# Kernel tuning notes

Measured on AMD Instinct MI355X. Metric: run time of the kernel, lower is better.

## Reference

```python
import jax, jax.numpy as jnp
import numpy as np

NEG_SLOPE = 0.2  # PyG GATConv default negative_slope
EPS = 1e-16      # PyG softmax denominator eps


def gat_layer(x, src, dst, W, a_src, a_dst, num_nodes):
    """One GATConv (eval mode, self-loops already appended to src/dst).
    x: [N, Fin], W: [Fin, H*C], a_src/a_dst: [H, C]. Returns [N, H, C]."""
    H, C = a_src.shape
    h = (x @ W).reshape(num_nodes, H, C)                  # [N,H,C]
    alpha_src = jnp.sum(h * a_src, axis=-1)               # [N,H]
    alpha_dst = jnp.sum(h * a_dst, axis=-1)               # [N,H]
    e = alpha_src[src] + alpha_dst[dst]                   # [E,H]
    e = jnp.where(e > 0, e, NEG_SLOPE * e)                # leaky_relu
    # segment softmax keyed by destination node
    m = jax.ops.segment_max(e, dst, num_segments=num_nodes)   # [N,H]
    ex = jnp.exp(e - m[dst])                              # [E,H]
    s = jax.ops.segment_sum(ex, dst, num_segments=num_nodes)  # [N,H]
    alpha = ex / (s[dst] + EPS)                           # [E,H]
    # weighted scatter-aggregation of source features
    msg = h[src] * alpha[..., None]                       # [E,H,C]
    out = jax.ops.segment_sum(msg, dst, num_segments=num_nodes)  # [N,H,C]
    return out


def setup_inputs() -> dict:
    key = jax.random.key(0)
    ks = jax.random.split(key, 10)
    N, E = 50000, 800000
    Fin, C1, H, Fout = 128, 32, 8, 1
    x = jax.random.normal(ks[0], (N, Fin), dtype=jnp.float32)
    edge_index = jax.random.randint(ks[1], (2, E), 0, N).astype(jnp.int64)
    sc = 0.1
    W1 = jax.random.normal(ks[2], (Fin, H * C1), dtype=jnp.float32) * sc
    att_src1 = jax.random.normal(ks[3], (H, C1), dtype=jnp.float32) * sc
    att_dst1 = jax.random.normal(ks[4], (H, C1), dtype=jnp.float32) * sc
    bias1 = jnp.zeros((H * C1,), dtype=jnp.float32)
    W2 = jax.random.normal(ks[5], (H * C1, Fout), dtype=jnp.float32) * sc
    att_src2 = jax.random.normal(ks[6], (1, Fout), dtype=jnp.float32) * sc
    att_dst2 = jax.random.normal(ks[7], (1, Fout), dtype=jnp.float32) * sc
    bias2 = jnp.zeros((Fout,), dtype=jnp.float32)
    return {"x": x, "edge_index": edge_index, "W1": W1, "att_src1": att_src1,
            "att_dst1": att_dst1, "bias1": bias1, "W2": W2, "att_src2": att_src2,
            "att_dst2": att_dst2, "bias2": bias2}


def reference(x, edge_index, W1, att_src1, att_dst1, bias1, W2, att_src2, att_dst2, bias2):
    N = x.shape[0]
    loops = jnp.arange(N, dtype=edge_index.dtype)
    src = jnp.concatenate([edge_index[0], loops])   # add_self_loops=True
    dst = jnp.concatenate([edge_index[1], loops])
    # layer 1: heads=8, concat=True
    h1 = gat_layer(x, src, dst, W1, att_src1, att_dst1, N)      # [N,H,C1]
    h1 = h1.reshape(N, -1) + bias1                               # [N,H*C1]
    h1 = jax.nn.elu(h1)
    # layer 2: heads=1, concat=False (single head -> identity mean)
    h2 = gat_layer(h1, src, dst, W2, att_src2, att_dst2, N)      # [N,1,1]
    h2 = h2.reshape(N, -1) + bias2                               # [N,1]
    return jax.nn.sigmoid(h2).squeeze(-1)                        # [N]
```

## Files before the change

### kernel.cpp

```cpp
#include <hip/hip_runtime.h>
#include <math.h>

#define NEG_SLOPE 0.2f
#define GAT_EPS 1e-16f
#define NEG_BIG -3.0e38f
#define LOG2E 1.4426950408889634f
#define MAXDEG 96
#define BCAP 6144
#define CHUNK 2048
#define PREPB 136

typedef __attribute__((ext_vector_type(8))) short short8;
typedef __attribute__((ext_vector_type(4))) float floatx4;

__device__ __forceinline__ float leaky(float v) {
    return v > 0.f ? v : NEG_SLOPE * v;
}
__device__ __forceinline__ unsigned short f2bf(float f) {
    unsigned u = __float_as_uint(f);
    unsigned r = u + 0x7FFFu + ((u >> 16) & 1u);
    return (unsigned short)(r >> 16);
}
__device__ __forceinline__ float bf2f(unsigned short h) {
    return __uint_as_float(((unsigned)h) << 16);
}

__global__ __launch_bounds__(256) void prep_scatterA(
    const float* __restrict__ W1, const float* __restrict__ a_src,
    const float* __restrict__ a_dst, unsigned short* __restrict__ w1t,
    const int* __restrict__ ei, unsigned int* __restrict__ bucket_buf,
    int* __restrict__ bucket_cnt, int E, int ET)
{
    __shared__ int lhist[256];
    __shared__ int lbase[256];
    const int t = threadIdx.x;

    if (blockIdx.x < PREPB) {
        int idx = blockIdx.x * 256 + t;
        if (idx < 128 * 256) {
            int n = idx >> 7, k = idx & 127;
            w1t[idx] = f2bf(W1[(size_t)k * 256 + n]);
        }
        if (idx < 2048) {
            int j = idx >> 7, k = idx & 127;
            const float* a = (j < 8) ? (a_src + j * 32) : (a_dst + (j - 8) * 32);
            const float* wr = W1 + (size_t)k * 256 + (j & 7) * 32;
            float s = 0.f;
            #pragma unroll
            for (int c = 0; c < 32; ++c) s += wr[c] * a[c];
            w1t[(size_t)(256 + j) * 128 + k] = f2bf(s);
        }
        return;
    }

    lhist[t] = 0;
    __syncthreads();
    const int base = (blockIdx.x - PREPB) * CHUNK;
    unsigned int pk[8]; int bk[8], rk[8]; bool v[8];
    #pragma unroll
    for (int k = 0; k < 8; ++k) {
        int i = base + k * 256 + t;
        v[k] = i < ET;
        int ii = v[k] ? i : 0;
        int src = (ii < E) ? ei[ii] : (ii - E);
        int dst = (ii < E) ? ei[E + ii] : (ii - E);
        bk[k] = dst >> 8;
        pk[k] = ((unsigned)src << 8) | (unsigned)(dst & 255);
    }
    #pragma unroll
    for (int k = 0; k < 8; ++k)
        if (v[k]) rk[k] = atomicAdd(&lhist[bk[k]], 1);
    __syncthreads();
    if (lhist[t] > 0) lbase[t] = atomicAdd(&bucket_cnt[t], lhist[t]);
    __syncthreads();
    #pragma unroll
    for (int k = 0; k < 8; ++k) {
        if (v[k]) {
            int pos = lbase[bk[k]] + rk[k];
            if (pos < BCAP) bucket_buf[(size_t)bk[k] * BCAP + pos] = pk[k];
        }
    }
}

__global__ __launch_bounds__(256) void gemm_scatterB(
    const float* __restrict__ x, const unsigned short* __restrict__ w1t,
    unsigned short* __restrict__ h1b, float* __restrict__ as1, float* __restrict__ ad1,
    const unsigned int* __restrict__ bucket_buf, const int* __restrict__ bucket_cnt,
    int* __restrict__ cnt, unsigned short* __restrict__ csr_pad,
    int N, int ntiles)
{
    __shared__ __align__(16) unsigned short Asl[64][40];
    __shared__ __align__(16) unsigned short Bsl[272][40];
    __shared__ int lcnt[256];
    const int t = threadIdx.x;

    if (blockIdx.x >= ntiles) {
        const int b = blockIdx.x - ntiles;
        lcnt[t] = 0;
        __syncthreads();
        int tot = bucket_cnt[b]; if (tot > BCAP) tot = BCAP;
        const unsigned int* bp = bucket_buf + (size_t)b * BCAP;
        for (int j = t; j < tot; j += 256) {
            unsigned int e = bp[j];
            int loc = e & 255;
            int src = (int)(e >> 8);
            int slot = atomicAdd(&lcnt[loc], 1);
            if (slot < MAXDEG)
                csr_pad[(((size_t)b << 8) | loc) * MAXDEG + slot] = (unsigned short)src;
        }
        __syncthreads();
        int node = (b << 8) | t;
        if (node < N) cnt[node] = lcnt[t];
        return;
    }

    const int row0 = blockIdx.x * 64;
    const int wave = t >> 6, lane = t & 63;
    const int l15 = lane & 15, quad = lane >> 4;

    floatx4 acc[17];
    #pragma unroll
    for (int i = 0; i < 17; ++i) acc[i] = (floatx4){0.f, 0.f, 0.f, 0.f};

    for (int kc = 0; kc < 128; kc += 32) {
        {
            int r = t >> 2, q = t & 3;
            int row = row0 + r; if (row > N - 1) row = N - 1;
            const float4* xp = (const float4*)(x + (size_t)row * 128 + kc + q * 8);
            float4 f0 = xp[0], f1 = xp[1];
            ushort4 u0, u1;
            u0.x = f2bf(f0.x); u0.y = f2bf(f0.y); u0.z = f2bf(f0.z); u0.w = f2bf(f0.w);
            u1.x = f2bf(f1.x); u1.y = f2bf(f1.y); u1.z = f2bf(f1.z); u1.w = f2bf(f1.w);
            *(ushort4*)&Asl[r][q * 8] = u0;
            *(ushort4*)&Asl[r][q * 8 + 4] = u1;
        }
        {
            #pragma unroll
            for (int q = 0; q < 4; ++q) {
                uint4 v = *(const uint4*)&w1t[(size_t)t * 128 + kc + q * 8];
                *(uint4*)&Bsl[t][q * 8] = v;
            }
            if (t < 16) {
                #pragma unroll
                for (int q = 0; q < 4; ++q) {
                    uint4 v = *(const uint4*)&w1t[(size_t)(256 + t) * 128 + kc + q * 8];
                    *(uint4*)&Bsl[256 + t][q * 8] = v;
                }
            }
        }
        __syncthreads();
        short8 a = *(const short8*)&Asl[wave * 16 + l15][quad * 8];
        #pragma unroll
        for (int nt = 0; nt < 17; ++nt) {
            short8 bb = *(const short8*)&Bsl[nt * 16 + l15][quad * 8];
            acc[nt] = __builtin_amdgcn_mfma_f32_16x16x32_bf16(a, bb, acc[nt], 0, 0, 0);
        }
        __syncthreads();
    }
    #pragma unroll
    for (int reg = 0; reg < 4; ++reg) {
        int row = row0 + wave * 16 + quad * 4 + reg;
        if (row < N) {
            #pragma unroll
            for (int nt = 0; nt < 16; ++nt) {
                int hh = nt >> 1, cc = ((nt & 1) << 4) + l15;
                h1b[((size_t)hh * N + row) * 32 + cc] = f2bf(acc[nt][reg]);
            }
            float vv = acc[16][reg] * LOG2E;
            if (l15 < 8) as1[(size_t)l15 * N + row] = vv;
            else         ad1[(size_t)(l15 - 8) * N + row] = vv;
        }
    }
}

__global__ __launch_bounds__(256) void aggr1_fused(
    const int* __restrict__ cnt, const unsigned short* __restrict__ csr_pad,
    const float* __restrict__ as1, const float* __restrict__ ad1,
    const unsigned short* __restrict__ h1b,
    const float* __restrict__ bias1, const float* __restrict__ W2,
    float* __restrict__ h2, int N)
{
    const int h = blockIdx.x & 7;
    const int n = (blockIdx.x >> 3) * 32 + (threadIdx.x >> 3);
    const int lane8 = threadIdx.x & 7;
    if (n >= N) return;
    const int wbase = (threadIdx.x & 63) & ~7;

    const size_t rs = (size_t)n * MAXDEG;
    int deg = cnt[n]; if (deg > MAXDEG) deg = MAXDEG;
    const float* as1h = as1 + (size_t)h * N;
    const unsigned short* h1h = h1b + ((size_t)h * N) * 32;
    float adv = ad1[(size_t)h * N + n];

    float m = NEG_BIG, s = 0.f;
    float4 acc = make_float4(0.f, 0.f, 0.f, 0.f);

    for (int j0 = 0; j0 < deg; j0 += 8) {
        bool va = (j0 + lane8) < deg;
        int sv = 0;
        if (va) sv = csr_pad[rs + j0 + lane8];
        float l = NEG_BIG;
        if (va) l = leaky(as1h[sv] + adv);
        int srcs[8];
        #pragma unroll
        for (int j = 0; j < 8; ++j) srcs[j] = __shfl(sv, wbase + j);
        uint2 hv[8];
        #pragma unroll
        for (int j = 0; j < 8; ++j)
            hv[j] = *(const uint2*)&h1h[((unsigned)srcs[j] << 5) + (lane8 << 2)];
        float lj[8];
        #pragma unroll
        for (int j = 0; j < 8; ++j) lj[j] = __shfl(l, wbase + j);
        float Mc = fmaxf(fmaxf(fmaxf(lj[0], lj[1]), fmaxf(lj[2], lj[3])),
                         fmaxf(fmaxf(lj[4], lj[5]), fmaxf(lj[6], lj[7])));
        if (__any(Mc > m + 8.f)) {
            float mn = fmaxf(m, Mc);
            float sc = exp2f(m - mn);
            s *= sc; acc.x *= sc; acc.y *= sc; acc.z *= sc; acc.w *= sc;
            m = mn;
        }
        #pragma unroll
        for (int j = 0; j < 8; ++j) {
            float p = exp2f(lj[j] - m);
            s += p;
            unsigned d0 = hv[j].x, d1 = hv[j].y;
            acc.x += p * __uint_as_float(d0 << 16);
            acc.y += p * __uint_as_float(d0 & 0xFFFF0000u);
            acc.z += p * __uint_as_float(d1 << 16);
            acc.w += p * __uint_as_float(d1 & 0xFFFF0000u);
        }
    }

    float inv = 1.f / (s + GAT_EPS);
    acc.x *= inv; acc.y *= inv; acc.z *= inv; acc.w *= inv;

    int f = h * 32 + lane8 * 4;
    float4 b = *(const float4*)&bias1[f];
    acc.x += b.x; acc.y += b.y; acc.z += b.z; acc.w += b.w;
    acc.x = acc.x > 0.f ? acc.x : __expf(acc.x) - 1.f;
    acc.y = acc.y > 0.f ? acc.y : __expf(acc.y) - 1.f;
    acc.z = acc.z > 0.f ? acc.z : __expf(acc.z) - 1.f;
    acc.w = acc.w > 0.f ? acc.w : __expf(acc.w) - 1.f;
    float4 w = *(const float4*)&W2[f];
    float part = acc.x * w.x + acc.y * w.y + acc.z * w.z + acc.w * w.w;
    part += __shfl_xor(part, 1);
    part += __shfl_xor(part, 2);
    part += __shfl_xor(part, 4);
    if (lane8 == 0) atomicAdd(&h2[n], part);
}

__global__ __launch_bounds__(256) void layer2_fused(
    const int* __restrict__ cnt, const unsigned short* __restrict__ csr_pad,
    const float* __restrict__ h2, const float* __restrict__ a_s2,
    const float* __restrict__ a_d2, const float* __restrict__ bias2,
    float* __restrict__ out, int N)
{
    int n = blockIdx.x * 16 + (threadIdx.x >> 4);
    int sl = threadIdx.x & 15;
    if (n >= N) return;
    const size_t rs = (size_t)n * MAXDEG;
    int deg = cnt[n]; if (deg > MAXDEG) deg = MAXDEG;
    float asc = a_s2[0], adc = a_d2[0];
    float hdc = h2[n] * adc;

    int k0 = sl, k1 = sl + 16;
    float hs0 = 0.f, hs1 = 0.f;
    bool v0 = k0 < deg, v1 = k1 < deg;
    if (v0) hs0 = h2[csr_pad[rs + k0]];
    if (v1) hs1 = h2[csr_pad[rs + k1]];

    float m = NEG_BIG, s = 0.f;
    if (v0) { m = leaky(hs0 * asc + hdc); s = 1.f; }
    if (v1) {
        float l = leaky(hs1 * asc + hdc);
        if (l > m) { s = s * __expf(m - l) + 1.f; m = l; }
        else       { s += __expf(l - m); }
    }
    for (int k = sl + 32; k < deg; k += 16) {
        float hs = h2[csr_pad[rs + k]];
        float l = leaky(hs * asc + hdc);
        if (l > m) { s = s * __expf(m - l) + 1.f; m = l; }
        else       { s += __expf(l - m); }
    }
    #pragma unroll
    for (int mask = 1; mask < 16; mask <<= 1) {
        float mo = __shfl_xor(m, mask);
        float so = __shfl_xor(s, mask);
        float M = fmaxf(m, mo);
        s = s * __expf(m - M) + so * __expf(mo - M);
        m = M;
    }
    float inv = 1.f / (s + GAT_EPS);

    float acc = 0.f;
    if (v0) acc += __expf(leaky(hs0 * asc + hdc) - m) * hs0;
    if (v1) acc += __expf(leaky(hs1 * asc + hdc) - m) * hs1;
    for (int k = sl + 32; k < deg; k += 16) {
        float hs = h2[csr_pad[rs + k]];
        float l = leaky(hs * asc + hdc);
        acc += __expf(l - m) * hs;
    }
    #pragma unroll
    for (int mask = 1; mask < 16; mask <<= 1) acc += __shfl_xor(acc, mask);
    if (sl == 0) {
        float z = acc * inv + bias2[0];
        out[n] = 1.f / (1.f + __expf(-z));
    }
}

extern "C" void kernel_launch(void* const* d_in, const int* in_sizes, int n_in,
                              void* d_out, int out_size, void* d_ws, size_t ws_size,
                              hipStream_t stream)
{
    const float* x      = (const float*)d_in[0];
    const int*   ei     = (const int*)  d_in[1];
    const float* W1     = (const float*)d_in[2];
    const float* a_src1 = (const float*)d_in[3];
    const float* a_dst1 = (const float*)d_in[4];
    const float* bias1  = (const float*)d_in[5];
    const float* W2     = (const float*)d_in[6];
    const float* a_s2   = (const float*)d_in[7];
    const float* a_d2   = (const float*)d_in[8];
    const float* bias2  = (const float*)d_in[9];
    float* out = (float*)d_out;

    const int N  = in_sizes[0] / 128;
    const int E  = in_sizes[1] / 2;
    const int ET = E + N;
    const int ntiles   = (N + 63) / 64;
    const int nbuckets = (N + 255) >> 8;
    const int ablocks  = (ET + CHUNK - 1) / CHUNK;
    const int ngroups  = (N + 31) / 32;

    char* wsb = (char*)d_ws;
    size_t off = 0;
    auto walloc = [&](size_t bytes) -> void* {
        void* p = wsb + off;
        off += (bytes + 255) & ~(size_t)255;
        return p;
    };
    unsigned short* w1t     = (unsigned short*)walloc((size_t)272 * 128 * 2);
    unsigned short* h1b     = (unsigned short*)walloc((size_t)N * 256 * 2);
    float*          as1     = (float*)         walloc((size_t)N * 8 * 4);
    float*          ad1     = (float*)         walloc((size_t)N * 8 * 4);
    float*          h2      = (float*)         walloc((size_t)N * 4);
    int*            cnt     = (int*)           walloc((size_t)N * 4);
    unsigned short* csr_pad = (unsigned short*)walloc((size_t)N * MAXDEG * 2);
    int*            bucket_cnt = (int*)        walloc(256 * 4);
    unsigned int*   bucket_buf = (unsigned int*)walloc((size_t)nbuckets * BCAP * 4);

    hipMemsetAsync(bucket_cnt, 0, 256 * sizeof(int), stream);
    hipMemsetAsync(h2, 0, (size_t)N * sizeof(float), stream);

    prep_scatterA<<<PREPB + ablocks, 256, 0, stream>>>(W1, a_src1, a_dst1, w1t,
                                                       ei, bucket_buf, bucket_cnt, E, ET);

    gemm_scatterB<<<ntiles + nbuckets, 256, 0, stream>>>(x, w1t, h1b, as1, ad1,
                                                         bucket_buf, bucket_cnt,
                                                         cnt, csr_pad, N, ntiles);

    aggr1_fused<<<ngroups * 8, 256, 0, stream>>>(cnt, csr_pad, as1, ad1, h1b,
                                                 bias1, W2, h2, N);
    layer2_fused<<<(N + 15) / 16, 256, 0, stream>>>(cnt, csr_pad, h2,
                                                    a_s2, a_d2, bias2, out, N);
}
```

Before: 211.4 us.

## Bin nodes by degree class so aggregation waves process uniform-degree nodes

During CSR construction each node is placed into one of 13 degree classes (degree rounded up to multiples of 8) and compacted into per-class node lists. The layer-1 aggregation kernel then maps each wave to 8 nodes of the same class, so the edge loop runs a fixed trip count with no divergence between the 8-node subgroups. This targets load imbalance where a wave waits on its highest-degree node. In exchange it adds extra atomics and a scattered node-id write, and the aggregation kernel gains an indirect node lookup, which makes its h2 atomics and ad1 loads non-contiguous.

```diff
diff --git a/kernel.cpp b/kernel.cpp
--- a/kernel.cpp
+++ b/kernel.cpp
@@ -6,6 +6,7 @@
 #define NEG_BIG -3.0e38f
 #define LOG2E 1.4426950408889634f
 #define MAXDEG 96
+#define NCLASS 13
 #define BCAP 6144
 #define CHUNK 2048
 #define PREPB 136
@@ -87,16 +88,20 @@
     unsigned short* __restrict__ h1b, float* __restrict__ as1, float* __restrict__ ad1,
     const unsigned int* __restrict__ bucket_buf, const int* __restrict__ bucket_cnt,
     int* __restrict__ cnt, unsigned short* __restrict__ csr_pad,
+    int* __restrict__ class_cnt, int* __restrict__ class_arr,
     int N, int ntiles)
 {
     __shared__ __align__(16) unsigned short Asl[64][40];
     __shared__ __align__(16) unsigned short Bsl[272][40];
     __shared__ int lcnt[256];
+    __shared__ int lcls[NCLASS + 3];
+    __shared__ int lclsbase[NCLASS + 3];
     const int t = threadIdx.x;
 
     if (blockIdx.x >= ntiles) {
         const int b = blockIdx.x - ntiles;
         lcnt[t] = 0;
+        if (t < NCLASS) lcls[t] = 0;
         __syncthreads();
         int tot = bucket_cnt[b]; if (tot > BCAP) tot = BCAP;
         const unsigned int* bp = bucket_buf + (size_t)b * BCAP;
@@ -110,7 +115,17 @@
         }
         __syncthreads();
         int node = (b << 8) | t;
-        if (node < N) cnt[node] = lcnt[t];
+        int d = 0, cls = 0, lpos = 0;
+        if (node < N) {
+            d = lcnt[t]; if (d > MAXDEG) d = MAXDEG;
+            cnt[node] = d;
+            cls = (d + 7) >> 3;
+            lpos = atomicAdd(&lcls[cls], 1);
+        }
+        __syncthreads();
+        if (t < NCLASS && lcls[t] > 0) lclsbase[t] = atomicAdd(&class_cnt[t], lcls[t]);
+        __syncthreads();
+        if (node < N) class_arr[cls * N + lclsbase[cls] + lpos] = node;
         return;
     }
 
@@ -177,25 +192,45 @@
     const int* __restrict__ cnt, const unsigned short* __restrict__ csr_pad,
     const float* __restrict__ as1, const float* __restrict__ ad1,
     const unsigned short* __restrict__ h1b,
+    const int* __restrict__ class_cnt, const int* __restrict__ class_arr,
     const float* __restrict__ bias1, const float* __restrict__ W2,
     float* __restrict__ h2, int N)
 {
     const int h = blockIdx.x & 7;
-    const int n = (blockIdx.x >> 3) * 32 + (threadIdx.x >> 3);
+    const int g = (blockIdx.x >> 3) * 4 + (threadIdx.x >> 6);
     const int lane8 = threadIdx.x & 7;
-    if (n >= N) return;
+    const int sub = (threadIdx.x >> 3) & 7;
     const int wbase = (threadIdx.x & 63) & ~7;
 
-    const size_t rs = (size_t)n * MAXDEG;
-    int deg = cnt[n]; if (deg > MAXDEG) deg = MAXDEG;
+    int c = -1, base = 0, ccnt = 0;
+    {
+        int pref = 0;
+        #pragma unroll
+        for (int k = 1; k < NCLASS; ++k) {
+            int nk = class_cnt[k];
+            int gk = (nk + 7) >> 3;
+            if (c < 0) {
+                if (g < pref + gk) { c = k; base = (g - pref) * 8; ccnt = nk; }
+                pref += gk;
+            }
+        }
+    }
+    if (c < 0) return;
+
+    const int idx = base + sub;
+    const bool uvalid = idx < ccnt;
+    const int nid = uvalid ? class_arr[c * N + idx] : 0;
+    const int deg = uvalid ? cnt[nid] : 0;
+    const size_t rs = (size_t)nid * MAXDEG;
     const float* as1h = as1 + (size_t)h * N;
     const unsigned short* h1h = h1b + ((size_t)h * N) * 32;
-    float adv = ad1[(size_t)h * N + n];
+    const float adv = ad1[(size_t)h * N + nid];
 
     float m = NEG_BIG, s = 0.f;
     float4 acc = make_float4(0.f, 0.f, 0.f, 0.f);
 
-    for (int j0 = 0; j0 < deg; j0 += 8) {
+    const int jend = c * 8;
+    for (int j0 = 0; j0 < jend; j0 += 8) {
         bool va = (j0 + lane8) < deg;
         int sv = 0;
         if (va) sv = csr_pad[rs + j0 + lane8];
@@ -246,7 +281,7 @@
     part += __shfl_xor(part, 1);
     part += __shfl_xor(part, 2);
     part += __shfl_xor(part, 4);
-    if (lane8 == 0) atomicAdd(&h2[n], part);
+    if (uvalid && lane8 == 0) atomicAdd(&h2[nid], part);
 }
 
 __global__ __launch_bounds__(256) void layer2_fused(
@@ -330,7 +365,7 @@
     const int ntiles   = (N + 63) / 64;
     const int nbuckets = (N + 255) >> 8;
     const int ablocks  = (ET + CHUNK - 1) / CHUNK;
-    const int ngroups  = (N + 31) / 32;
+    const int gmax     = (N + 7) / 8 + NCLASS;
 
     char* wsb = (char*)d_ws;
     size_t off = 0;
@@ -346,10 +381,12 @@
     float*          h2      = (float*)         walloc((size_t)N * 4);
     int*            cnt     = (int*)           walloc((size_t)N * 4);
     unsigned short* csr_pad = (unsigned short*)walloc((size_t)N * MAXDEG * 2);
-    int*            bucket_cnt = (int*)        walloc(256 * 4);
+    int*            bucket_cnt = (int*)        walloc((256 + 16) * 4);
+    int*            class_cnt  = bucket_cnt + 256;
+    int*            class_arr  = (int*)        walloc(((size_t)NCLASS * N + 256) * 4);
     unsigned int*   bucket_buf = (unsigned int*)walloc((size_t)nbuckets * BCAP * 4);
 
-    hipMemsetAsync(bucket_cnt, 0, 256 * sizeof(int), stream);
+    hipMemsetAsync(bucket_cnt, 0, (256 + 16) * sizeof(int), stream);
     hipMemsetAsync(h2, 0, (size_t)N * sizeof(float), stream);
 
     prep_scatterA<<<PREPB + ablocks, 256, 0, stream>>>(W1, a_src1, a_dst1, w1t,
@@ -357,10 +394,13 @@
 
     gemm_scatterB<<<ntiles + nbuckets, 256, 0, stream>>>(x, w1t, h1b, as1, ad1,
                                                          bucket_buf, bucket_cnt,
-                                                         cnt, csr_pad, N, ntiles);
-
-    aggr1_fused<<<ngroups * 8, 256, 0, stream>>>(cnt, csr_pad, as1, ad1, h1b,
-                                                 bias1, W2, h2, N);
+                                                         cnt, csr_pad,
+                                                         class_cnt, class_arr,
+                                                         N, ntiles);
+
+    aggr1_fused<<<8 * ((gmax + 3) / 4), 256, 0, stream>>>(cnt, csr_pad, as1, ad1, h1b,
+                                                          class_cnt, class_arr,
+                                                          bias1, W2, h2, N);
     layer2_fused<<<(N + 15) / 16, 256, 0, stream>>>(cnt, csr_pad, h2,
                                                     a_s2, a_d2, bias2, out, N);
 }
```

Result: no change. 210.9 us (-0.2%).
